# Performance work log

Measured on AMD Instinct MI355X. Metric: run time of the kernel, lower is better.

Reference implementation:

```python
import jax, jax.numpy as jnp
import numpy as np

B, S, T = 32, 512, 128   # batch, source chars, target (protoform) chars
V, L = 128, 5            # char vocab len(C2I), number of languages
E, H, F = 512, 1024, 2048  # embedding_dim, model_size, feedforward_dim
START_CHAR, SEP_LANG = 1, L - 1


def setup_inputs() -> dict:
    key = jax.random.key(0)
    ks = jax.random.split(key, 32)
    f32 = jnp.float32

    def n(k, shape, fan_in):
        return jax.random.normal(k, shape, dtype=f32) * (1.0 / np.sqrt(fan_in))

    inp = {
        "src_chars": jax.random.randint(ks[0], (B, S), 0, V),
        "src_langs": jax.random.randint(ks[1], (B, S), 0, L),
        "tgt_chars": jax.random.randint(ks[2], (B, T), 0, V),
        # embedding feature extractor
        "char_emb": jax.random.normal(ks[3], (V, E), dtype=f32) * 0.02,
        "lang_emb": jax.random.normal(ks[4], (L, E), dtype=f32) * 0.02,
        "fc_W": n(ks[5], (E, 2 * E), 2 * E),
        "fc_b": jnp.zeros((E,), f32),
        # encoder GRU (PyTorch gate layout r,z,n)
        "enc_Wi": n(ks[6], (3 * H, E), E),
        "enc_Wh": n(ks[7], (3 * H, H), H),
        "enc_bi": jnp.zeros((3 * H,), f32),
        "enc_bh": jnp.zeros((3 * H,), f32),
        # decoder GRU, input = [E ; H]
        "dec_Wi": n(ks[8], (3 * H, E + H), E + H),
        "dec_Wh": n(ks[9], (3 * H, H), H),
        "dec_bi": jnp.zeros((3 * H,), f32),
        "dec_bh": jnp.zeros((3 * H,), f32),
        # attention
        "Wq": n(ks[10], (H, H), H),
        "Wk": n(ks[11], (H, H), H),
        "Wcs": n(ks[12], (H, E), E),
        # MLP H -> 2F -> F -> V
        "W1": n(ks[13], (2 * F, H), H),
        "b1": jnp.zeros((2 * F,), f32),
        "W2": n(ks[14], (F, 2 * F), 2 * F),
        "b2": jnp.zeros((F,), f32),
        "W3": n(ks[15], (V, F), F),
    }
    return inp


def _gru_step(h, x, Wi, Wh, bi, bh):
    gi = x @ Wi.T + bi            # [B, 3H]
    gh = h @ Wh.T + bh            # [B, 3H]
    ir, iz, inn = jnp.split(gi, 3, axis=-1)
    hr, hz, hn = jnp.split(gh, 3, axis=-1)
    r = jax.nn.sigmoid(ir + hr)
    z = jax.nn.sigmoid(iz + hz)
    n = jnp.tanh(inn + r * hn)
    return (1.0 - z) * n + z * h


def _mlp(x, W1, b1, W2, b2, W3):
    h = jax.nn.relu(x @ W1.T + b1)
    h = jax.nn.relu(h @ W2.T + b2)
    return h @ W3.T               # [B, V]


def reference(src_chars, src_langs, tgt_chars,
              char_emb, lang_emb, fc_W, fc_b,
              enc_Wi, enc_Wh, enc_bi, enc_bh,
              dec_Wi, dec_Wh, dec_bi, dec_bh,
              Wq, Wk, Wcs,
              W1, b1, W2, b2, W3):
    # --- feature extraction: concat(char_emb, lang_emb) -> Linear(2E -> E) ---
    def embed(c_idx, l_idx):
        ce = char_emb[c_idx]                       # [..., E]
        le = lang_emb[l_idx]                       # [..., E]
        return jnp.concatenate([ce, le], -1) @ fc_W.T + fc_b

    encoded = embed(src_chars, src_langs)          # [B, S, E]

    # --- encoder GRU over source chars ---
    def enc_step(h, x_t):
        h = _gru_step(h, x_t, enc_Wi, enc_Wh, enc_bi, enc_bh)
        return h, h

    h0 = jnp.zeros((encoded.shape[0], enc_Wh.shape[1]), encoded.dtype)
    _, enc_states = jax.lax.scan(enc_step, h0, jnp.swapaxes(encoded, 0, 1))
    enc_states = jnp.swapaxes(enc_states, 0, 1)    # [B, S, H]

    # precompute attention values: W_c_s(encoded) + W_key(keys)  [B, S, H]
    att_vals = encoded @ Wcs.T + enc_states @ Wk.T

    # --- initial decoder step: <s> embedding + last encoder state ---
    start_emb = embed(jnp.full((encoded.shape[0],), START_CHAR),
                      jnp.full((encoded.shape[0],), SEP_LANG))  # [B, E]
    context0 = enc_states[:, -1]                   # [B, H]
    d0 = jnp.zeros_like(context0)
    dec_h = _gru_step(d0, jnp.concatenate([start_emb, context0], -1),
                      dec_Wi, dec_Wh, dec_bi, dec_bh)

    tgt_emb = embed(tgt_chars, jnp.full_like(tgt_chars, SEP_LANG))  # [B, T, E]

    # --- decode T steps with teacher forcing ---
    def dec_step(carry, x_t):
        h, ctx = carry
        scores_t = _mlp(h + ctx, W1, b1, W2, b2, W3)           # [B, V]
        q = h @ Wq.T                                           # [B, H]
        att = jnp.einsum('bsh,bh->bs', enc_states, q)
        w = jax.nn.softmax(att, axis=-1)
        ctx_new = jnp.einsum('bs,bsh->bh', w, att_vals)        # [B, H]
        h_new = _gru_step(h, jnp.concatenate([x_t, ctx_new], -1),
                          dec_Wi, dec_Wh, dec_bi, dec_bh)
        return (h_new, ctx_new), scores_t

    (_, _), scores = jax.lax.scan(dec_step, (dec_h, context0),
                                  jnp.swapaxes(tgt_emb, 0, 1))
    return jnp.swapaxes(scores, 0, 1)              # [B, T, V]
```

## Files before the change

kernel.cpp:

```cpp
#include <hip/hip_runtime.h>
#include <math.h>


#define Bb 32
#define Ss 512
#define Tt 128
#define Vv 128
#define Hh 1024
#define H3 3072
#define APAD 40
#define NBE 64
#define NBD 128

typedef __attribute__((ext_vector_type(8))) short bf16x8;
typedef __attribute__((ext_vector_type(4))) float f32x4;

__device__ inline f32x4 mfma_bf16(bf16x8 a, bf16x8 b, f32x4 c) {
  return __builtin_amdgcn_mfma_f32_16x16x32_bf16(a, b, c, 0, 0, 0);
}
__device__ inline unsigned short f2bf(float f) {
  unsigned u = __builtin_bit_cast(unsigned, f);
  unsigned r = (u + 0x7fffu + ((u >> 16) & 1u)) >> 16;
  return (unsigned short)r;
}
__device__ inline float lof(unsigned u) { return __builtin_bit_cast(float, u << 16); }
__device__ inline float hif(unsigned u) { return __builtin_bit_cast(float, u & 0xffff0000u); }
__device__ inline float bf2f(unsigned short h) {
  return __builtin_bit_cast(float, ((unsigned)h) << 16);
}

#define O_ESBF   0UL
#define O_ESQ    33554432UL
#define O_AVBF   67108864UL
#define O_HCBF   100663296UL
#define O_WHE    109051904UL
#define O_WHD    115343360UL
#define O_WIC    121634816UL
#define O_WKB    127926272UL
#define O_WQT    130023424UL
#define O_W1B    132120576UL
#define O_W2B    140509184UL
#define O_W3B    157286400UL
#define O_XCAT   157810688UL
#define O_EMBFC  160432128UL
#define O_GITAB  161742848UL
#define O_AVTAB  169607168UL
#define O_DGIXT  172228608UL
#define O_GH     173801472UL
#define O_GI     174194688UL
#define O_H      174587904UL
#define O_HBF    174718976UL
#define O_CTX    174784512UL
#define O_CTXBF  174915584UL
#define O_ATTL   174981120UL

__global__ void k_xcat(const float* __restrict__ ce, const float* __restrict__ le,
                       float* __restrict__ xcat) {
  int row = blockIdx.x;
  int l = row >> 7, c = row & 127;
  int i = threadIdx.x * 4;
  float4 v;
  if (i < 512) v = *(const float4*)(ce + c * 512 + i);
  else         v = *(const float4*)(le + l * 512 + (i - 512));
  *(float4*)(xcat + (size_t)row * 1024 + i) = v;
}

__global__ void k_cltab(const int* __restrict__ sc, const int* __restrict__ sl,
                        int* __restrict__ cl, int* __restrict__ bar) {
  if (blockIdx.x == 0 && threadIdx.x < 256) bar[threadIdx.x] = 0;
  int i = blockIdx.x * 256 + threadIdx.x;
  int b = i >> 9, s = i & 511;
  cl[s * 32 + b] = sl[b * Ss + s] * 128 + sc[b * Ss + s];
}

__global__ void k_cvt(const float* __restrict__ src, int ld, int lc,
                      unsigned short* __restrict__ dst) {
  size_t i = ((size_t)blockIdx.x * 256 + threadIdx.x) * 8;
  size_t r = i >> lc;
  int c = (int)(i & ((1u << lc) - 1));
  const float* s = src + r * (size_t)ld + c;
  float4 v0 = *(const float4*)s;
  float4 v1 = *(const float4*)(s + 4);
  union { unsigned short us[8]; uint4 u; } o;
  o.us[0] = f2bf(v0.x); o.us[1] = f2bf(v0.y); o.us[2] = f2bf(v0.z); o.us[3] = f2bf(v0.w);
  o.us[4] = f2bf(v1.x); o.us[5] = f2bf(v1.y); o.us[6] = f2bf(v1.z); o.us[7] = f2bf(v1.w);
  *(uint4*)(dst + i) = o.u;
}

__global__ void k_transcvt(const float* __restrict__ in, unsigned short* __restrict__ out) {
  __shared__ float t[32][33];
  int c0 = blockIdx.x * 32, r0 = blockIdx.y * 32;
  int tx = threadIdx.x, ty = threadIdx.y;
  for (int i = ty; i < 32; i += 8)
    t[i][tx] = in[(size_t)(r0 + i) * 1024 + c0 + tx];
  __syncthreads();
  for (int i = ty; i < 32; i += 8)
    out[(size_t)(c0 + i) * 1024 + r0 + tx] = f2bf(t[tx][i]);
}

template <bool BIAS>
__global__ __launch_bounds__(256) void k_gemm(
    const float* __restrict__ A, int lda, const float* __restrict__ W, int ldw,
    const float* __restrict__ bias, float* __restrict__ C, int ldc, int K) {
  __shared__ float As[8][128];
  __shared__ float Ws[8][128];
  int tid = threadIdx.x;
  int n0 = blockIdx.x * 128, m0 = blockIdx.y * 128;
  int tx = tid & 15, ty = tid >> 4;
  int lrow = tid >> 1, lseg = (tid & 1) * 4;
  const float* Ap = A + (size_t)(m0 + lrow) * lda + lseg;
  const float* Wp = W + (size_t)(n0 + lrow) * ldw + lseg;
  float acc[8][8];
#pragma unroll
  for (int i = 0; i < 8; ++i)
#pragma unroll
    for (int j = 0; j < 8; ++j) acc[i][j] = 0.f;
  for (int kt = 0; kt < K; kt += 8) {
    float4 av = *(const float4*)(Ap + kt);
    float4 wv = *(const float4*)(Wp + kt);
    __syncthreads();
    As[lseg + 0][lrow] = av.x; As[lseg + 1][lrow] = av.y;
    As[lseg + 2][lrow] = av.z; As[lseg + 3][lrow] = av.w;
    Ws[lseg + 0][lrow] = wv.x; Ws[lseg + 1][lrow] = wv.y;
    Ws[lseg + 2][lrow] = wv.z; Ws[lseg + 3][lrow] = wv.w;
    __syncthreads();
#pragma unroll
    for (int kk = 0; kk < 8; ++kk) {
      float a[8], b[8];
      *(float4*)(a + 0) = *(const float4*)(&As[kk][ty * 8 + 0]);
      *(float4*)(a + 4) = *(const float4*)(&As[kk][ty * 8 + 4]);
      *(float4*)(b + 0) = *(const float4*)(&Ws[kk][tx * 8 + 0]);
      *(float4*)(b + 4) = *(const float4*)(&Ws[kk][tx * 8 + 4]);
#pragma unroll
      for (int i = 0; i < 8; ++i)
#pragma unroll
        for (int j = 0; j < 8; ++j) acc[i][j] = fmaf(a[i], b[j], acc[i][j]);
    }
  }
#pragma unroll
  for (int i = 0; i < 8; ++i) {
    int r = m0 + ty * 8 + i;
#pragma unroll
    for (int j = 0; j < 8; ++j) {
      int c = n0 + tx * 8 + j;
      float v = acc[i][j];
      if (BIAS) v += bias[c];
      C[(size_t)r * ldc + c] = v;
    }
  }
}

template <int EPI, bool RELU, bool BIAS>
__global__ __launch_bounds__(256) void k_bgemm(
    const unsigned short* __restrict__ A, int lda,
    const unsigned short* __restrict__ W, int ldw,
    const float* __restrict__ bias, void* __restrict__ Cout, int ldc, int K,
    const float* __restrict__ avtab, const int* __restrict__ gl,
    const int* __restrict__ gc) {
  __shared__ unsigned short As[128 * APAD];
  __shared__ unsigned short Bs[128 * APAD];
  int tid = threadIdx.x;
  int n0 = blockIdx.x * 128, m0 = blockIdx.y * 128;
  int w = tid >> 6, l = tid & 63;
  int mw = (w & 1) * 64, nw = (w >> 1) * 64;
  int lrow = tid >> 1, lk = (tid & 1) * 16;
  const unsigned short* Ap = A + (size_t)(m0 + lrow) * lda + lk;
  const unsigned short* Wp = W + (size_t)(n0 + lrow) * ldw + lk;
  int fr = l & 15, fk = (l >> 4) * 8;
  f32x4 acc[4][4];
#pragma unroll
  for (int i = 0; i < 4; ++i)
#pragma unroll
    for (int j = 0; j < 4; ++j) acc[i][j] = (f32x4){0.f, 0.f, 0.f, 0.f};
  for (int kt = 0; kt < K; kt += 32) {
    uint4 a0 = *(const uint4*)(Ap + kt);
    uint4 a1 = *(const uint4*)(Ap + kt + 8);
    uint4 b0 = *(const uint4*)(Wp + kt);
    uint4 b1 = *(const uint4*)(Wp + kt + 8);
    __syncthreads();
    *(uint4*)&As[lrow * APAD + lk] = a0;
    *(uint4*)&As[lrow * APAD + lk + 8] = a1;
    *(uint4*)&Bs[lrow * APAD + lk] = b0;
    *(uint4*)&Bs[lrow * APAD + lk + 8] = b1;
    __syncthreads();
    bf16x8 af[4], bfg[4];
#pragma unroll
    for (int i = 0; i < 4; ++i) af[i] = *(const bf16x8*)&As[(mw + i * 16 + fr) * APAD + fk];
#pragma unroll
    for (int j = 0; j < 4; ++j) bfg[j] = *(const bf16x8*)&Bs[(nw + j * 16 + fr) * APAD + fk];
#pragma unroll
    for (int i = 0; i < 4; ++i)
#pragma unroll
      for (int j = 0; j < 4; ++j) acc[i][j] = mfma_bf16(af[i], bfg[j], acc[i][j]);
  }
#pragma unroll
  for (int i = 0; i < 4; ++i)
#pragma unroll
    for (int j = 0; j < 4; ++j) {
      int col = n0 + nw + j * 16 + fr;
#pragma unroll
      for (int r = 0; r < 4; ++r) {
        int row = m0 + mw + i * 16 + (l >> 4) * 4 + r;
        float v = acc[i][j][r];
        if (BIAS) v += bias[col];
        if (RELU) v = fmaxf(v, 0.f);
        if (EPI == 0) {
          ((unsigned short*)Cout)[(size_t)row * ldc + col] = f2bf(v);
        } else if (EPI == 1) {
          int cl = gl[row] * 128 + gc[row];
          ((unsigned short*)Cout)[(size_t)row * ldc + col] =
              f2bf(v + avtab[(size_t)cl * 1024 + col]);
        } else {
          int tt = row >> 5, bb = row & 31;
          ((float*)Cout)[(size_t)bb * (Tt * Vv) + tt * Vv + col] = v;
        }
      }
    }
}

__global__ __launch_bounds__(512) void k_enc_pers(
    const unsigned short* __restrict__ Whe, const float* __restrict__ gitab,
    const int* __restrict__ cltab, const float* __restrict__ bh,
    float* __restrict__ h, unsigned short* __restrict__ hbf0,
    unsigned short* __restrict__ hbf1, unsigned short* __restrict__ esb,
    int* __restrict__ bar) {
  __shared__ unsigned short Ws[48 * 1024];
  __shared__ f32x4 red[8 * 6 * 64];
  int tid = threadIdx.x;
  int blk = blockIdx.x;
  int w = tid >> 6, l = tid & 63;
  int fr = l & 15, q = l >> 4;
  int j = blk * 16 + fr;
  {
    uint4* dst = (uint4*)Ws;
    const uint4* src = (const uint4*)Whe;
#pragma unroll
    for (int it = 0; it < 12; ++it) {
      int idx = it * 512 + tid;
      int lr = idx >> 7, c = idx & 127;
      int grow = (lr >> 4) * 1024 + blk * 16 + (lr & 15);
      dst[lr * 128 + (c ^ (lr & 7))] = src[(size_t)grow * 128 + c];
    }
  }
  float bhr = bh[j], bhz = bh[1024 + j], bhn = bh[2048 + j];
  float hold[4] = {0.f, 0.f, 0.f, 0.f};
  __syncthreads();
  const bf16x8* Wsv = (const bf16x8*)Ws;
  int bc = 0;
  for (int s = 0; s < Ss; ++s) {
    unsigned short* wb = (s & 1) ? hbf1 : hbf0;
    const unsigned short* rb = (s & 1) ? hbf0 : hbf1;
    float gi0[4], gi1[4], gi2[4];
    if (w < 2) {
#pragma unroll
      for (int r = 0; r < 4; ++r) {
        int b = w * 16 + q * 4 + r;
        int c = cltab[s * 32 + b];
        const float* gp = gitab + (size_t)c * H3 + j;
        gi0[r] = gp[0]; gi1[r] = gp[1024]; gi2[r] = gp[2048];
      }
    }
    f32x4 acc[2][3];
#pragma unroll
    for (int m = 0; m < 2; ++m)
#pragma unroll
      for (int g = 0; g < 3; ++g) acc[m][g] = (f32x4){0.f, 0.f, 0.f, 0.f};
    if (s > 0) {
      int kb = w * 128 + q * 8;
      const unsigned short* A0 = rb + fr * 1024 + kb;
#pragma unroll
      for (int kt = 0; kt < 128; kt += 32) {
        bf16x8 a0 = *(const bf16x8*)(A0 + kt);
        bf16x8 a1 = *(const bf16x8*)(A0 + 16 * 1024 + kt);
        int c8 = (kb + kt) >> 3;
#pragma unroll
        for (int g = 0; g < 3; ++g) {
          bf16x8 bw = Wsv[(g * 16 + fr) * 128 + (c8 ^ (fr & 7))];
          acc[0][g] = mfma_bf16(a0, bw, acc[0][g]);
          acc[1][g] = mfma_bf16(a1, bw, acc[1][g]);
        }
      }
    }
#pragma unroll
    for (int m = 0; m < 2; ++m)
#pragma unroll
      for (int g = 0; g < 3; ++g)
        red[(w * 6 + m * 3 + g) * 64 + l] = acc[m][g];
    __syncthreads();
    if (w < 2) {
      int m = w;
      f32x4 as_[3];
#pragma unroll
      for (int g = 0; g < 3; ++g) as_[g] = (f32x4){0.f, 0.f, 0.f, 0.f};
#pragma unroll
      for (int ww = 0; ww < 8; ++ww)
#pragma unroll
        for (int g = 0; g < 3; ++g)
          as_[g] = as_[g] + red[(ww * 6 + m * 3 + g) * 64 + l];
#pragma unroll
      for (int r = 0; r < 4; ++r) {
        int b = m * 16 + q * 4 + r;
        float ghr = bhr + as_[0][r], ghz = bhz + as_[1][r], ghn = bhn + as_[2][r];
        float rg = 1.f / (1.f + expf(-(gi0[r] + ghr)));
        float zg = 1.f / (1.f + expf(-(gi1[r] + ghz)));
        float ng = tanhf(gi2[r] + rg * ghn);
        float hn = (1.f - zg) * ng + zg * hold[r];
        hold[r] = hn;
        unsigned short hb = f2bf(hn);
        wb[b * 1024 + j] = hb;
        esb[((size_t)b * Ss + s) * 1024 + j] = hb;
        if (s == Ss - 1) h[b * 1024 + j] = hn;
      }
    }
    __syncthreads();
    if (tid == 0) {
      __hip_atomic_fetch_add(bar, 1, __ATOMIC_RELEASE, __HIP_MEMORY_SCOPE_AGENT);
      ++bc;
      int tgt = NBE * bc;
      while (__hip_atomic_load(bar, __ATOMIC_RELAXED, __HIP_MEMORY_SCOPE_AGENT) < tgt)
        __builtin_amdgcn_s_sleep(1);
      __builtin_amdgcn_fence(__ATOMIC_ACQUIRE, "agent");
    }
    __syncthreads();
  }
}

__global__ __launch_bounds__(512) void k_dec_pers(
    const unsigned short* __restrict__ Whd, const unsigned short* __restrict__ Wic,
    const unsigned short* __restrict__ esq, const unsigned short* __restrict__ av,
    const float* __restrict__ dgixt, const int* __restrict__ tgt,
    const float* __restrict__ bh, float* __restrict__ h,
    unsigned short* __restrict__ hbf, float* __restrict__ ctx,
    unsigned short* __restrict__ ctxbf, float* __restrict__ attL,
    float* __restrict__ ghbuf, unsigned short* __restrict__ hcbf,
    int* __restrict__ bar) {
  __shared__ unsigned short Ws[48 * 1024];
  __shared__ float scr[12 * 1024];
  __shared__ float hs[1024];
  __shared__ float wS[512];
  __shared__ float wm[4], wsm[4];
  f32x4* red = (f32x4*)scr;
  int tid = threadIdx.x;
  int blk = blockIdx.x;
  int wv = tid >> 6, l = tid & 63;
  int fr = l & 15, q = l >> 4;
  int rnd = 0;
  bool isGH = blk < 64;
  int jsl = (blk & 63) * 16;
  {
    const uint4* src = (const uint4*)(isGH ? Whd : Wic);
    uint4* dst = (uint4*)Ws;
#pragma unroll
    for (int it = 0; it < 12; ++it) {
      int idx = it * 512 + tid;
      int lr = idx >> 7, c = idx & 127;
      int grow = (lr >> 4) * 1024 + jsl + (lr & 15);
      dst[lr * 128 + (c ^ (lr & 7))] = src[(size_t)grow * 128 + c];
    }
  }
  const bf16x8* Wsv = (const bf16x8*)Ws;
  int jw = jsl + fr;
  float bhr = bh[jw], bhz = bh[1024 + jw], bhn = bh[2048 + jw];
  int batch = (blk - 64) >> 1, hf = (blk - 64) & 1;
  int b2 = blk >> 2, jq = blk & 3;

#define GBAR()                                                                          \
  do {                                                                                  \
    __syncthreads();                                                                    \
    if (tid == 0) {                                                                     \
      ++rnd;                                                                            \
      int gl_ = (blk >> 5) * 16;                                                        \
      int old_ = __hip_atomic_fetch_add(&bar[gl_], 1, __ATOMIC_RELEASE,                 \
                                        __HIP_MEMORY_SCOPE_AGENT);                      \
      if (old_ == rnd * 32 - 1)                                                         \
        __hip_atomic_fetch_add(&bar[64], 1, __ATOMIC_RELEASE,                           \
                               __HIP_MEMORY_SCOPE_AGENT);                               \
      while (__hip_atomic_load(&bar[64], __ATOMIC_RELAXED,                              \
                               __HIP_MEMORY_SCOPE_AGENT) < rnd * 4)                     \
        __builtin_amdgcn_s_sleep(1);                                                    \
      __builtin_amdgcn_fence(__ATOMIC_ACQUIRE, "agent");                                \
    }                                                                                   \
    __syncthreads();                                                                    \
  } while (0)

  if (tid < 256) {
    int idx = blk * 256 + tid;
    float v = h[idx];
    ctx[idx] = v;
    ctxbf[idx] = f2bf(v);
  }
  GBAR();
  if (!isGH) {
    f32x4 acc[2][3];
#pragma unroll
    for (int m = 0; m < 2; ++m)
#pragma unroll
      for (int g = 0; g < 3; ++g) acc[m][g] = (f32x4){0.f, 0.f, 0.f, 0.f};
    int kb = wv * 128 + q * 8;
    const unsigned short* A0 = ctxbf + fr * 1024 + kb;
#pragma unroll
    for (int kt = 0; kt < 128; kt += 32) {
      bf16x8 a0 = *(const bf16x8*)(A0 + kt);
      bf16x8 a1 = *(const bf16x8*)(A0 + 16 * 1024 + kt);
      int c8 = (kb + kt) >> 3;
#pragma unroll
      for (int g = 0; g < 3; ++g) {
        bf16x8 bw = Wsv[(g * 16 + fr) * 128 + (c8 ^ (fr & 7))];
        acc[0][g] = mfma_bf16(a0, bw, acc[0][g]);
        acc[1][g] = mfma_bf16(a1, bw, acc[1][g]);
      }
    }
#pragma unroll
    for (int m = 0; m < 2; ++m)
#pragma unroll
      for (int g = 0; g < 3; ++g)
        red[(wv * 6 + m * 3 + g) * 64 + l] = acc[m][g];
    __syncthreads();
    if (wv < 2) {
      int m = wv;
      f32x4 as_[3];
#pragma unroll
      for (int g = 0; g < 3; ++g) as_[g] = (f32x4){0.f, 0.f, 0.f, 0.f};
#pragma unroll
      for (int ww = 0; ww < 8; ++ww)
#pragma unroll
        for (int g = 0; g < 3; ++g)
          as_[g] = as_[g] + red[(ww * 6 + m * 3 + g) * 64 + l];
      const float* gp = dgixt + (size_t)1 * H3 + jw;
#pragma unroll
      for (int r = 0; r < 4; ++r) {
        int b = m * 16 + q * 4 + r;
        float gir = gp[0] + as_[0][r];
        float giz = gp[1024] + as_[1][r];
        float gin = gp[2048] + as_[2][r];
        float rg = 1.f / (1.f + expf(-(gir + bhr)));
        float zg = 1.f / (1.f + expf(-(giz + bhz)));
        float ng = tanhf(gin + rg * bhn);
        float hn = (1.f - zg) * ng;
        h[b * 1024 + jw] = hn;
        hbf[b * 1024 + jw] = f2bf(hn);
      }
    }
  }
  GBAR();
  for (int t = 0; t < Tt; ++t) {
    if (isGH) {
      f32x4 acc[2][3];
#pragma unroll
      for (int m = 0; m < 2; ++m)
#pragma unroll
        for (int g = 0; g < 3; ++g) acc[m][g] = (f32x4){0.f, 0.f, 0.f, 0.f};
      int kb = wv * 128 + q * 8;
      const unsigned short* A0 = hbf + fr * 1024 + kb;
#pragma unroll
      for (int kt = 0; kt < 128; kt += 32) {
        bf16x8 a0 = *(const bf16x8*)(A0 + kt);
        bf16x8 a1 = *(const bf16x8*)(A0 + 16 * 1024 + kt);
        int c8 = (kb + kt) >> 3;
#pragma unroll
        for (int g = 0; g < 3; ++g) {
          bf16x8 bw = Wsv[(g * 16 + fr) * 128 + (c8 ^ (fr & 7))];
          acc[0][g] = mfma_bf16(a0, bw, acc[0][g]);
          acc[1][g] = mfma_bf16(a1, bw, acc[1][g]);
        }
      }
#pragma unroll
      for (int m = 0; m < 2; ++m)
#pragma unroll
        for (int g = 0; g < 3; ++g)
          red[(wv * 6 + m * 3 + g) * 64 + l] = acc[m][g];
      __syncthreads();
      if (wv < 2) {
        int m = wv;
        f32x4 as_[3];
#pragma unroll
        for (int g = 0; g < 3; ++g) as_[g] = (f32x4){0.f, 0.f, 0.f, 0.f};
#pragma unroll
        for (int ww = 0; ww < 8; ++ww)
#pragma unroll
          for (int g = 0; g < 3; ++g)
            as_[g] = as_[g] + red[(ww * 6 + m * 3 + g) * 64 + l];
#pragma unroll
        for (int r = 0; r < 4; ++r) {
          int b = m * 16 + q * 4 + r;
#pragma unroll
          for (int g = 0; g < 3; ++g)
            ghbuf[b * H3 + g * 1024 + jw] = as_[g][r];
        }
      }
    } else {
      for (int i = tid; i < 1024; i += 512) hs[i] = h[batch * 1024 + i];
      __syncthreads();
      {
        int j2 = hf * 512 + tid;
        hcbf[(size_t)t * (Bb * Hh) + batch * 1024 + j2] =
            f2bf(hs[j2] + ctx[batch * 1024 + j2]);
      }
      int sg = tid >> 2, li = tid & 3;
      int s0 = hf * 256 + sg;
      const unsigned short* ep0 = esq + (size_t)(batch * 512 + s0) * 1024;
      const unsigned short* ep1 = ep0 + 128 * 1024;
      float acc0 = 0.f, acc1 = 0.f;
#pragma unroll 4
      for (int i = 0; i < 32; ++i) {
        int k = (i * 4 + li) * 8;
        uint4 e0 = *(const uint4*)(ep0 + k);
        uint4 e1 = *(const uint4*)(ep1 + k);
        float4 h0 = *(const float4*)&hs[k];
        float4 h1 = *(const float4*)&hs[k + 4];
        acc0 += lof(e0.x) * h0.x + hif(e0.x) * h0.y + lof(e0.y) * h0.z + hif(e0.y) * h0.w +
                lof(e0.z) * h1.x + hif(e0.z) * h1.y + lof(e0.w) * h1.z + hif(e0.w) * h1.w;
        acc1 += lof(e1.x) * h0.x + hif(e1.x) * h0.y + lof(e1.y) * h0.z + hif(e1.y) * h0.w +
                lof(e1.z) * h1.x + hif(e1.z) * h1.y + lof(e1.w) * h1.z + hif(e1.w) * h1.w;
      }
      acc0 += __shfl_xor(acc0, 1);
      acc0 += __shfl_xor(acc0, 2);
      acc1 += __shfl_xor(acc1, 1);
      acc1 += __shfl_xor(acc1, 2);
      if (li == 0) {
        attL[batch * 512 + s0] = acc0;
        attL[batch * 512 + s0 + 128] = acc1;
      }
    }
    if (t == Tt - 1) break;
    GBAR();
    {
      float a0 = 0.f, a1 = 0.f;
      if (tid < 256) {
        a0 = attL[b2 * Ss + tid * 2];
        a1 = attL[b2 * Ss + tid * 2 + 1];
        float m = fmaxf(a0, a1);
        for (int d = 1; d < 64; d <<= 1) m = fmaxf(m, __shfl_xor(m, d));
        if ((tid & 63) == 0) wm[tid >> 6] = m;
      }
      __syncthreads();
      if (tid < 256) {
        float m = fmaxf(fmaxf(wm[0], wm[1]), fmaxf(wm[2], wm[3]));
        float e0 = expf(a0 - m), e1 = expf(a1 - m);
        wS[tid * 2] = e0;
        wS[tid * 2 + 1] = e1;
        float ssum = e0 + e1;
        for (int d = 1; d < 64; d <<= 1) ssum += __shfl_xor(ssum, d);
        if ((tid & 63) == 0) wsm[tid >> 6] = ssum;
      }
      __syncthreads();
      float scale = 1.f / (wsm[0] + wsm[1] + wsm[2] + wsm[3]);
      int g = tid & 31, si = tid >> 5;
      const unsigned short* avp = av + (size_t)(b2 * 512) * 1024 + jq * 256 + g * 8;
      float a8[8] = {0.f, 0.f, 0.f, 0.f, 0.f, 0.f, 0.f, 0.f};
#pragma unroll 4
      for (int s = si; s < 512; s += 16) {
        float wv2 = wS[s];
        uint4 e = *(const uint4*)(avp + (size_t)s * 1024);
        a8[0] += wv2 * lof(e.x); a8[1] += wv2 * hif(e.x);
        a8[2] += wv2 * lof(e.y); a8[3] += wv2 * hif(e.y);
        a8[4] += wv2 * lof(e.z); a8[5] += wv2 * hif(e.z);
        a8[6] += wv2 * lof(e.w); a8[7] += wv2 * hif(e.w);
      }
      __syncthreads();
#pragma unroll
      for (int k2 = 0; k2 < 8; ++k2) scr[tid * 8 + k2] = a8[k2];
      __syncthreads();
      if (tid < 256) {
        float p = 0.f;
#pragma unroll
        for (int si2 = 0; si2 < 16; ++si2) p += scr[si2 * 256 + tid];
        float v = p * scale;
        int j3 = b2 * 1024 + jq * 256 + tid;
        ctx[j3] = v;
        ctxbf[j3] = f2bf(v);
      }
    }
    GBAR();
    if (!isGH) {
      f32x4 acc[2][3];
#pragma unroll
      for (int m = 0; m < 2; ++m)
#pragma unroll
        for (int g = 0; g < 3; ++g) acc[m][g] = (f32x4){0.f, 0.f, 0.f, 0.f};
      int kb = wv * 128 + q * 8;
      const unsigned short* A0 = ctxbf + fr * 1024 + kb;
#pragma unroll
      for (int kt = 0; kt < 128; kt += 32) {
        bf16x8 a0 = *(const bf16x8*)(A0 + kt);
        bf16x8 a1 = *(const bf16x8*)(A0 + 16 * 1024 + kt);
        int c8 = (kb + kt) >> 3;
#pragma unroll
        for (int g = 0; g < 3; ++g) {
          bf16x8 bw = Wsv[(g * 16 + fr) * 128 + (c8 ^ (fr & 7))];
          acc[0][g] = mfma_bf16(a0, bw, acc[0][g]);
          acc[1][g] = mfma_bf16(a1, bw, acc[1][g]);
        }
      }
#pragma unroll
      for (int m = 0; m < 2; ++m)
#pragma unroll
        for (int g = 0; g < 3; ++g)
          red[(wv * 6 + m * 3 + g) * 64 + l] = acc[m][g];
      __syncthreads();
      if (wv < 2) {
        int m = wv;
        f32x4 as_[3];
#pragma unroll
        for (int g = 0; g < 3; ++g) as_[g] = (f32x4){0.f, 0.f, 0.f, 0.f};
#pragma unroll
        for (int ww = 0; ww < 8; ++ww)
#pragma unroll
          for (int g = 0; g < 3; ++g)
            as_[g] = as_[g] + red[(ww * 6 + m * 3 + g) * 64 + l];
#pragma unroll
        for (int r = 0; r < 4; ++r) {
          int b = m * 16 + q * 4 + r;
          int c = tgt[b * Tt + t];
          const float* gp = dgixt + (size_t)c * H3 + jw;
          float gir = gp[0] + as_[0][r];
          float giz = gp[1024] + as_[1][r];
          float gin = gp[2048] + as_[2][r];
          const float* g2 = ghbuf + b * H3 + jw;
          float ghr = bhr + g2[0];
          float ghz = bhz + g2[1024];
          float ghn = bhn + g2[2048];
          float rg = 1.f / (1.f + expf(-(gir + ghr)));
          float zg = 1.f / (1.f + expf(-(giz + ghz)));
          float ng = tanhf(gin + rg * ghn);
          float hn = (1.f - zg) * ng + zg * h[b * 1024 + jw];
          h[b * 1024 + jw] = hn;
          hbf[b * 1024 + jw] = f2bf(hn);
        }
      }
    }
    GBAR();
  }
#undef GBAR
}

extern "C" void kernel_launch(void* const* d_in, const int* in_sizes, int n_in,
                              void* d_out, int out_size, void* d_ws, size_t ws_size,
                              hipStream_t stream) {
  (void)in_sizes; (void)n_in; (void)out_size; (void)ws_size;
  const int*   src_chars = (const int*)d_in[0];
  const int*   src_langs = (const int*)d_in[1];
  const int*   tgt_chars = (const int*)d_in[2];
  const float* char_emb  = (const float*)d_in[3];
  const float* lang_emb  = (const float*)d_in[4];
  const float* fc_W  = (const float*)d_in[5];
  const float* fc_b  = (const float*)d_in[6];
  const float* enc_Wi = (const float*)d_in[7];
  const float* enc_Wh = (const float*)d_in[8];
  const float* enc_bi = (const float*)d_in[9];
  const float* enc_bh = (const float*)d_in[10];
  const float* dec_Wi = (const float*)d_in[11];
  const float* dec_Wh = (const float*)d_in[12];
  const float* dec_bi = (const float*)d_in[13];
  const float* dec_bh = (const float*)d_in[14];
  const float* Wq  = (const float*)d_in[15];
  const float* Wk  = (const float*)d_in[16];
  const float* Wcs = (const float*)d_in[17];
  const float* W1 = (const float*)d_in[18];
  const float* b1 = (const float*)d_in[19];
  const float* W2 = (const float*)d_in[20];
  const float* b2 = (const float*)d_in[21];
  const float* W3 = (const float*)d_in[22];
  float* out = (float*)d_out;

  char* ws = (char*)d_ws;
  unsigned short* esbf  = (unsigned short*)(ws + O_ESBF);
  unsigned short* esq   = (unsigned short*)(ws + O_ESQ);
  unsigned short* avbf  = (unsigned short*)(ws + O_AVBF);
  unsigned short* hcbf  = (unsigned short*)(ws + O_HCBF);
  unsigned short* WheB  = (unsigned short*)(ws + O_WHE);
  unsigned short* WhdB  = (unsigned short*)(ws + O_WHD);
  unsigned short* WicB  = (unsigned short*)(ws + O_WIC);
  unsigned short* WkB   = (unsigned short*)(ws + O_WKB);
  unsigned short* WqTB  = (unsigned short*)(ws + O_WQT);
  unsigned short* W1B   = (unsigned short*)(ws + O_W1B);
  unsigned short* W2B   = (unsigned short*)(ws + O_W2B);
  unsigned short* W3B   = (unsigned short*)(ws + O_W3B);
  float* xcat   = (float*)(ws + O_XCAT);
  float* embfc  = (float*)(ws + O_EMBFC);
  float* gitab  = (float*)(ws + O_GITAB);
  float* avtab  = (float*)(ws + O_AVTAB);
  float* dgixt  = (float*)(ws + O_DGIXT);
  float* ghbuf  = (float*)(ws + O_GH);
  float* h      = (float*)(ws + O_H);
  unsigned short* hbf   = (unsigned short*)(ws + O_HBF);
  float* ctx    = (float*)(ws + O_CTX);
  unsigned short* ctxbf = (unsigned short*)(ws + O_CTXBF);
  float* attL   = (float*)(ws + O_ATTL);
  unsigned short* G1 = esq;
  unsigned short* G2 = avbf;
  int* cltab = (int*)(ws + O_GI);
  unsigned short* hbf2 = (unsigned short*)(ws + O_GI + 65536);
  int* bar = (int*)(ws + O_GI + 131072);

  dim3 blk(256);

  k_xcat<<<640, blk, 0, stream>>>(char_emb, lang_emb, xcat);
  k_cltab<<<64, blk, 0, stream>>>(src_chars, src_langs, cltab, bar);
  k_gemm<true><<<dim3(4, 5), blk, 0, stream>>>(xcat, 1024, fc_W, 1024, fc_b, embfc, 512, 1024);
  k_gemm<true><<<dim3(24, 5), blk, 0, stream>>>(embfc, 512, enc_Wi, 512, enc_bi, gitab, H3, 512);
  k_gemm<false><<<dim3(8, 5), blk, 0, stream>>>(embfc, 512, Wcs, 512, nullptr, avtab, Hh, 512);
  k_gemm<true><<<dim3(24, 1), blk, 0, stream>>>(embfc + 512 * 512, 512, dec_Wi, 1536, dec_bi,
                                                dgixt, H3, 512);
  k_cvt<<<1536, blk, 0, stream>>>(enc_Wh, 1024, 10, WheB);
  k_cvt<<<1536, blk, 0, stream>>>(dec_Wh, 1024, 10, WhdB);
  k_cvt<<<1536, blk, 0, stream>>>(dec_Wi + 512, 1536, 10, WicB);
  k_cvt<<<512,  blk, 0, stream>>>(Wk, 1024, 10, WkB);
  k_cvt<<<2048, blk, 0, stream>>>(W1, 1024, 10, W1B);
  k_cvt<<<4096, blk, 0, stream>>>(W2, 4096, 12, W2B);
  k_cvt<<<128,  blk, 0, stream>>>(W3, 2048, 11, W3B);
  k_transcvt<<<dim3(32, 32), dim3(32, 8), 0, stream>>>(Wq, WqTB);

  {
    const unsigned short* p_whe = WheB;
    const float* p_git = gitab;
    const int* p_cl = cltab;
    const float* p_bh = enc_bh;
    float* p_h = h;
    unsigned short* p_h0 = hbf;
    unsigned short* p_h1 = hbf2;
    unsigned short* p_esb = esbf;
    int* p_bar = bar + 128;
    void* kargs[] = {(void*)&p_whe, (void*)&p_git, (void*)&p_cl, (void*)&p_bh,
                     (void*)&p_h, (void*)&p_h0, (void*)&p_h1, (void*)&p_esb,
                     (void*)&p_bar};
    hipLaunchCooperativeKernel((const void*)k_enc_pers, dim3(NBE), dim3(512), kargs, 0, stream);
  }

  k_bgemm<0, false, false><<<dim3(8, 128), blk, 0, stream>>>(
      esbf, 1024, WqTB, 1024, nullptr, esq, 1024, 1024, nullptr, nullptr, nullptr);
  k_bgemm<1, false, false><<<dim3(8, 128), blk, 0, stream>>>(
      esbf, 1024, WkB, 1024, nullptr, avbf, 1024, 1024, avtab, src_langs, src_chars);

  {
    const unsigned short* p_whd = WhdB;
    const unsigned short* p_wic = WicB;
    const unsigned short* p_esq = esq;
    const unsigned short* p_av = avbf;
    const float* p_dgixt = dgixt;
    const int* p_tgt = tgt_chars;
    const float* p_bh = dec_bh;
    float* p_h = h;
    unsigned short* p_hbf = hbf;
    float* p_ctx = ctx;
    unsigned short* p_ctxbf = ctxbf;
    float* p_attL = attL;
    float* p_gh = ghbuf;
    unsigned short* p_hc = hcbf;
    int* p_bar = bar;
    void* kargs[] = {(void*)&p_whd, (void*)&p_wic, (void*)&p_esq, (void*)&p_av,
                     (void*)&p_dgixt, (void*)&p_tgt, (void*)&p_bh, (void*)&p_h,
                     (void*)&p_hbf, (void*)&p_ctx, (void*)&p_ctxbf, (void*)&p_attL,
                     (void*)&p_gh, (void*)&p_hc, (void*)&p_bar};
    hipLaunchCooperativeKernel((const void*)k_dec_pers, dim3(NBD), dim3(512), kargs, 0, stream);
  }

  k_bgemm<0, true, true><<<dim3(32, 32), blk, 0, stream>>>(
      hcbf, 1024, W1B, 1024, b1, G1, 4096, 1024, nullptr, nullptr, nullptr);
  k_bgemm<0, true, true><<<dim3(16, 32), blk, 0, stream>>>(
      G1, 4096, W2B, 4096, b2, G2, 2048, 4096, nullptr, nullptr, nullptr);
  k_bgemm<2, false, false><<<dim3(1, 32), blk, 0, stream>>>(
      G2, 2048, W3B, 2048, nullptr, out, 0, 2048, nullptr, nullptr, nullptr);
}
```

Baseline: 9.208 ms.

## Use flag-based grid barriers and spread decoder attention over twice as many blocks

Both persistent kernels now use a grid barrier where each block writes its own padded arrival flag and block 0 gathers them, then releases eight go flags. This replaces the contended fetch-add counters. The decoder grid grows from 128 to 256 blocks, and the attention-score and context work is spread across more blocks: 4 blocks per batch for scores, and 8 column slices per batch for context. More blocks means more parallelism for those bandwidth-bound phases, at the cost of a heavier barrier with more participants and a serial gather in block 0.

```diff
diff --git a/kernel.cpp b/kernel.cpp
--- a/kernel.cpp
+++ b/kernel.cpp
@@ -10,7 +10,7 @@
 #define H3 3072
 #define APAD 40
 #define NBE 64
-#define NBD 128
+#define NBD 256
 
 typedef __attribute__((ext_vector_type(8))) short bf16x8;
 typedef __attribute__((ext_vector_type(4))) float f32x4;
@@ -54,6 +54,8 @@
 #define O_CTXBF  174915584UL
 #define O_ATTL   174981120UL
 
+#define BAR_N 5376
+
 __global__ void k_xcat(const float* __restrict__ ce, const float* __restrict__ le,
                        float* __restrict__ xcat) {
   int row = blockIdx.x;
@@ -67,7 +69,9 @@
 
 __global__ void k_cltab(const int* __restrict__ sc, const int* __restrict__ sl,
                         int* __restrict__ cl, int* __restrict__ bar) {
-  if (blockIdx.x == 0 && threadIdx.x < 256) bar[threadIdx.x] = 0;
+  if (blockIdx.x == 0) {
+    for (int i2 = threadIdx.x; i2 < BAR_N; i2 += 256) bar[i2] = 0;
+  }
   int i = blockIdx.x * 256 + threadIdx.x;
   int b = i >> 9, s = i & 511;
   cl[s * 32 + b] = sl[b * Ss + s] * 128 + sc[b * Ss + s];
@@ -226,6 +230,8 @@
     int* __restrict__ bar) {
   __shared__ unsigned short Ws[48 * 1024];
   __shared__ f32x4 red[8 * 6 * 64];
+  int* earr = bar;
+  int* ego  = bar + 1024;
   int tid = threadIdx.x;
   int blk = blockIdx.x;
   int w = tid >> 6, l = tid & 63;
@@ -313,11 +319,25 @@
       }
     }
     __syncthreads();
+    ++bc;
+    if (tid == 0)
+      __hip_atomic_store(&earr[blk * 16], bc, __ATOMIC_RELEASE, __HIP_MEMORY_SCOPE_AGENT);
+    if (blk == 0) {
+      if (tid < NBE) {
+        while (__hip_atomic_load(&earr[tid * 16], __ATOMIC_RELAXED,
+                                 __HIP_MEMORY_SCOPE_AGENT) < bc)
+          __builtin_amdgcn_s_sleep(1);
+      }
+      __syncthreads();
+      if (tid == 0) {
+        __builtin_amdgcn_fence(__ATOMIC_ACQUIRE, "agent");
+        for (int x = 0; x < 8; ++x)
+          __hip_atomic_store(&ego[x * 16], bc, __ATOMIC_RELEASE, __HIP_MEMORY_SCOPE_AGENT);
+      }
+    }
     if (tid == 0) {
-      __hip_atomic_fetch_add(bar, 1, __ATOMIC_RELEASE, __HIP_MEMORY_SCOPE_AGENT);
-      ++bc;
-      int tgt = NBE * bc;
-      while (__hip_atomic_load(bar, __ATOMIC_RELAXED, __HIP_MEMORY_SCOPE_AGENT) < tgt)
+      while (__hip_atomic_load(&ego[(blk & 7) * 16], __ATOMIC_RELAXED,
+                               __HIP_MEMORY_SCOPE_AGENT) < bc)
         __builtin_amdgcn_s_sleep(1);
       __builtin_amdgcn_fence(__ATOMIC_ACQUIRE, "agent");
     }
@@ -340,14 +360,17 @@
   __shared__ float wS[512];
   __shared__ float wm[4], wsm[4];
   f32x4* red = (f32x4*)scr;
+  int* darr = bar;
+  int* dgo  = bar + 4096;
   int tid = threadIdx.x;
   int blk = blockIdx.x;
   int wv = tid >> 6, l = tid & 63;
   int fr = l & 15, q = l >> 4;
   int rnd = 0;
   bool isGH = blk < 64;
+  bool isGI = (blk >= 64 && blk < 128);
   int jsl = (blk & 63) * 16;
-  {
+  if (blk < 128) {
     const uint4* src = (const uint4*)(isGH ? Whd : Wic);
     uint4* dst = (uint4*)Ws;
 #pragma unroll
@@ -361,36 +384,47 @@
   const bf16x8* Wsv = (const bf16x8*)Ws;
   int jw = jsl + fr;
   float bhr = bh[jw], bhz = bh[1024 + jw], bhn = bh[2048 + jw];
-  int batch = (blk - 64) >> 1, hf = (blk - 64) & 1;
-  int b2 = blk >> 2, jq = blk & 3;
+  int batch = (blk - 128) >> 2, aq = (blk - 128) & 3;
+  int b2 = blk >> 3, jq = blk & 7;
 
 #define GBAR()                                                                          \
   do {                                                                                  \
     __syncthreads();                                                                    \
+    ++rnd;                                                                              \
+    if (tid == 0)                                                                       \
+      __hip_atomic_store(&darr[blk * 16], rnd, __ATOMIC_RELEASE,                        \
+                         __HIP_MEMORY_SCOPE_AGENT);                                     \
+    if (blk == 0) {                                                                     \
+      if (tid < NBD) {                                                                  \
+        while (__hip_atomic_load(&darr[tid * 16], __ATOMIC_RELAXED,                     \
+                                 __HIP_MEMORY_SCOPE_AGENT) < rnd)                       \
+          __builtin_amdgcn_s_sleep(1);                                                  \
+      }                                                                                 \
+      __syncthreads();                                                                  \
+      if (tid == 0) {                                                                   \
+        __builtin_amdgcn_fence(__ATOMIC_ACQUIRE, "agent");                              \
+        for (int x = 0; x < 8; ++x)                                                     \
+          __hip_atomic_store(&dgo[x * 16], rnd, __ATOMIC_RELEASE,                       \
+                             __HIP_MEMORY_SCOPE_AGENT);                                 \
+      }                                                                                 \
+    }                                                                                   \
     if (tid == 0) {                                                                     \
-      ++rnd;                                                                            \
-      int gl_ = (blk >> 5) * 16;                                                        \
-      int old_ = __hip_atomic_fetch_add(&bar[gl_], 1, __ATOMIC_RELEASE,                 \
-                                        __HIP_MEMORY_SCOPE_AGENT);                      \
-      if (old_ == rnd * 32 - 1)                                                         \
-        __hip_atomic_fetch_add(&bar[64], 1, __ATOMIC_RELEASE,                           \
-                               __HIP_MEMORY_SCOPE_AGENT);                               \
-      while (__hip_atomic_load(&bar[64], __ATOMIC_RELAXED,                              \
-                               __HIP_MEMORY_SCOPE_AGENT) < rnd * 4)                     \
+      while (__hip_atomic_load(&dgo[(blk & 7) * 16], __ATOMIC_RELAXED,                  \
+                               __HIP_MEMORY_SCOPE_AGENT) < rnd)                         \
         __builtin_amdgcn_s_sleep(1);                                                    \
       __builtin_amdgcn_fence(__ATOMIC_ACQUIRE, "agent");                                \
     }                                                                                   \
     __syncthreads();                                                                    \
   } while (0)
 
-  if (tid < 256) {
+  if (blk < 128 && tid < 256) {
     int idx = blk * 256 + tid;
     float v = h[idx];
     ctx[idx] = v;
     ctxbf[idx] = f2bf(v);
   }
   GBAR();
-  if (!isGH) {
+  if (isGI) {
     f32x4 acc[2][3];
 #pragma unroll
     for (int m = 0; m < 2; ++m)
@@ -488,39 +522,30 @@
             ghbuf[b * H3 + g * 1024 + jw] = as_[g][r];
         }
       }
-    } else {
+    } else if (blk >= 128) {
       for (int i = tid; i < 1024; i += 512) hs[i] = h[batch * 1024 + i];
       __syncthreads();
-      {
-        int j2 = hf * 512 + tid;
+      if (tid < 256) {
+        int j2 = aq * 256 + tid;
         hcbf[(size_t)t * (Bb * Hh) + batch * 1024 + j2] =
             f2bf(hs[j2] + ctx[batch * 1024 + j2]);
       }
       int sg = tid >> 2, li = tid & 3;
-      int s0 = hf * 256 + sg;
+      int s0 = aq * 128 + sg;
       const unsigned short* ep0 = esq + (size_t)(batch * 512 + s0) * 1024;
-      const unsigned short* ep1 = ep0 + 128 * 1024;
-      float acc0 = 0.f, acc1 = 0.f;
-#pragma unroll 4
+      float acc0 = 0.f;
+#pragma unroll 8
       for (int i = 0; i < 32; ++i) {
         int k = (i * 4 + li) * 8;
         uint4 e0 = *(const uint4*)(ep0 + k);
-        uint4 e1 = *(const uint4*)(ep1 + k);
         float4 h0 = *(const float4*)&hs[k];
         float4 h1 = *(const float4*)&hs[k + 4];
         acc0 += lof(e0.x) * h0.x + hif(e0.x) * h0.y + lof(e0.y) * h0.z + hif(e0.y) * h0.w +
                 lof(e0.z) * h1.x + hif(e0.z) * h1.y + lof(e0.w) * h1.z + hif(e0.w) * h1.w;
-        acc1 += lof(e1.x) * h0.x + hif(e1.x) * h0.y + lof(e1.y) * h0.z + hif(e1.y) * h0.w +
-                lof(e1.z) * h1.x + hif(e1.z) * h1.y + lof(e1.w) * h1.z + hif(e1.w) * h1.w;
       }
       acc0 += __shfl_xor(acc0, 1);
       acc0 += __shfl_xor(acc0, 2);
-      acc1 += __shfl_xor(acc1, 1);
-      acc1 += __shfl_xor(acc1, 2);
-      if (li == 0) {
-        attL[batch * 512 + s0] = acc0;
-        attL[batch * 512 + s0 + 128] = acc1;
-      }
+      if (li == 0) attL[batch * 512 + s0] = acc0;
     }
     if (t == Tt - 1) break;
     GBAR();
@@ -545,11 +570,11 @@
       }
       __syncthreads();
       float scale = 1.f / (wsm[0] + wsm[1] + wsm[2] + wsm[3]);
-      int g = tid & 31, si = tid >> 5;
-      const unsigned short* avp = av + (size_t)(b2 * 512) * 1024 + jq * 256 + g * 8;
+      int g = tid & 15, si = tid >> 4;
+      const unsigned short* avp = av + (size_t)(b2 * 512) * 1024 + jq * 128 + g * 8;
       float a8[8] = {0.f, 0.f, 0.f, 0.f, 0.f, 0.f, 0.f, 0.f};
 #pragma unroll 4
-      for (int s = si; s < 512; s += 16) {
+      for (int s = si; s < 512; s += 32) {
         float wv2 = wS[s];
         uint4 e = *(const uint4*)(avp + (size_t)s * 1024);
         a8[0] += wv2 * lof(e.x); a8[1] += wv2 * hif(e.x);
@@ -561,18 +586,19 @@
 #pragma unroll
       for (int k2 = 0; k2 < 8; ++k2) scr[tid * 8 + k2] = a8[k2];
       __syncthreads();
-      if (tid < 256) {
+      if (tid < 128) {
+        int g2 = tid >> 3, k2 = tid & 7;
         float p = 0.f;
 #pragma unroll
-        for (int si2 = 0; si2 < 16; ++si2) p += scr[si2 * 256 + tid];
+        for (int si2 = 0; si2 < 32; ++si2) p += scr[(si2 * 16 + g2) * 8 + k2];
         float v = p * scale;
-        int j3 = b2 * 1024 + jq * 256 + tid;
+        int j3 = b2 * 1024 + jq * 128 + tid;
         ctx[j3] = v;
         ctxbf[j3] = f2bf(v);
       }
     }
     GBAR();
-    if (!isGH) {
+    if (isGI) {
       f32x4 acc[2][3];
 #pragma unroll
       for (int m = 0; m < 2; ++m)
@@ -720,7 +746,7 @@
     unsigned short* p_h0 = hbf;
     unsigned short* p_h1 = hbf2;
     unsigned short* p_esb = esbf;
-    int* p_bar = bar + 128;
+    int* p_bar = bar + 4224;
     void* kargs[] = {(void*)&p_whe, (void*)&p_git, (void*)&p_cl, (void*)&p_bh,
                      (void*)&p_h, (void*)&p_h0, (void*)&p_h1, (void*)&p_esb,
                      (void*)&p_bar};
```

Result: slower. 12.66 ms (+37.5%).
